# Performance work log

Measured on AMD Instinct MI355X. Metric: run time of the kernel, lower is better.

The kernel has to match this reference:

```python
import jax, jax.numpy as jnp
import numpy as np

M = 8          # ensemble size
B = 16384      # batch
HIST = 5       # history
L = 384        # latent_dim
A = 1          # action_dim
HID = 512      # hidden_dim
NHL = 2        # num_hidden_layers
DIN = L * HIST + A * HIST  # 1925
EPS = 1e-5     # BatchNorm eps


def setup_inputs() -> dict:
    key = jax.random.key(0)
    ks = jax.random.split(key, 6)
    w = lambda k, shape: (jax.random.normal(k, shape, jnp.float32) * 0.02)
    return {
        "z_hist": jax.random.normal(ks[0], (B, HIST, L), jnp.float32),
        "a_hist": jax.random.normal(ks[1], (B, HIST, A), jnp.float32),
        # per-model parameters, stacked along leading ensemble dim M
        "W1": w(ks[2], (M, DIN, HID)),
        "b1": jnp.zeros((M, HID), jnp.float32),
        "Wh": w(ks[3], (NHL, M, HID, HID)),
        "bh": jnp.zeros((NHL, M, HID), jnp.float32),
        "gamma": jnp.ones((NHL, M, HID), jnp.float32),
        "beta": jnp.zeros((NHL, M, HID), jnp.float32),
        "rmean": jnp.zeros((NHL, M, HID), jnp.float32),   # BN running mean (eval mode)
        "rvar": jnp.ones((NHL, M, HID), jnp.float32),      # BN running var (eval mode)
        "W3": w(ks[4], (M, HID, L)),
        "b3": jnp.zeros((M, L), jnp.float32),
    }


def reference(z_hist, a_hist, W1, b1, Wh, bh, gamma, beta, rmean, rvar, W3, b3):
    # EnsembleTransitionModel.forward, batched over the ensemble dim instead of
    # a Python loop over models. BatchNorm in eval mode; Dropout inactive (eval).
    bsz = z_hist.shape[0]
    x = jnp.concatenate([z_hist.reshape(bsz, -1), a_hist.reshape(bsz, -1)], axis=1)  # [B, DIN]
    # input projection + ReLU: [M, B, HID]
    h = jax.nn.relu(jnp.einsum('bi,mih->mbh', x, W1) + b1[:, None, :])
    n_layers = Wh.shape[0]
    for l in range(n_layers):  # small fixed structural loop (num_hidden_layers)
        h = jnp.einsum('mbh,mhk->mbk', h, Wh[l]) + bh[l][:, None, :]
        h = (h - rmean[l][:, None, :]) * jax.lax.rsqrt(rvar[l][:, None, :] + EPS)
        h = jax.nn.relu(h * gamma[l][:, None, :] + beta[l][:, None, :])
    delta = jnp.einsum('mbh,mhl->mbl', h, W3) + b3[:, None, :]
    # residual: pred_z = z_t + delta, broadcast over ensemble dim
    return delta + z_hist[:, -1, :][None, :, :]
```

## Files before the change

### kernel.cpp

```cpp
#include <hip/hip_runtime.h>
#include <hip/hip_bf16.h>

#define M_ENS 8
#define BATCH 16384
#define HIST 5
#define LDIM 384
#define HID 512
#define NHL 2
#define DIN 1925
#define KP 1984
#define ZLEN (HIST * LDIM)

typedef unsigned short u16;
typedef unsigned int u32;
typedef unsigned long long u64;
typedef __attribute__((ext_vector_type(8))) short bf16x8;
typedef __attribute__((ext_vector_type(4))) float f32x4;

__device__ __forceinline__ u16 f2b(float f) {
    u32 u = __builtin_bit_cast(u32, f);
    u32 r = (u + 0x7fffu + ((u >> 16) & 1u)) >> 16;
    return (u16)r;
}

#define BARRIER asm volatile("s_barrier" ::: "memory")
#define GLL(src, dst) __builtin_amdgcn_global_load_lds( \
    (const __attribute__((address_space(1))) void*)(src), \
    (__attribute__((address_space(3))) void*)(dst), 16, 0, 0)

__global__ void build_x(const float* __restrict__ z, const float* __restrict__ a,
                        u16* __restrict__ xp) {
    int idx = blockIdx.x * 256 + threadIdx.x;
    int b = idx / (KP / 4);
    int k4 = (idx % (KP / 4)) * 4;
    if (b >= BATCH) return;
    u16 r[4];
    if (k4 + 4 <= ZLEN) {
        float4 v = *(const float4*)(z + (size_t)b * ZLEN + k4);
        r[0] = f2b(v.x); r[1] = f2b(v.y); r[2] = f2b(v.z); r[3] = f2b(v.w);
    } else {
#pragma unroll
        for (int j = 0; j < 4; ++j) {
            int k = k4 + j;
            float v = 0.f;
            if (k < ZLEN)      v = z[(size_t)b * ZLEN + k];
            else if (k < DIN)  v = a[b * HIST + (k - ZLEN)];
            r[j] = f2b(v);
        }
    }
    u64 pk = (u64)r[0] | ((u64)r[1] << 16) | ((u64)r[2] << 32) | ((u64)r[3] << 48);
    *(u64*)(&xp[(size_t)b * KP + k4]) = pk;
}

__global__ void transpose_cvt(const float* __restrict__ in, u16* __restrict__ out,
                              int R, int C, int Rp) {
    __shared__ float tile[32][33];
    const float* inb = in + (size_t)blockIdx.z * R * C;
    u16* outb = out + (size_t)blockIdx.z * C * Rp;
    int r0 = blockIdx.x * 32, c0 = blockIdx.y * 32;
    int tx = threadIdx.x & 31, ty = threadIdx.x >> 5;
#pragma unroll
    for (int i = 0; i < 32; i += 8) {
        int r = r0 + ty + i;
        float v = 0.f;
        if (r < R) v = inb[(size_t)r * C + c0 + tx];
        tile[ty + i][tx] = v;
    }
    __syncthreads();
#pragma unroll
    for (int i = 0; i < 32; i += 8) {
        outb[(size_t)(c0 + ty + i) * Rp + r0 + tx] = f2b(tile[tx][ty + i]);
    }
}

__global__ void make_tables(const float* __restrict__ bh, const float* __restrict__ gamma,
                            const float* __restrict__ beta, const float* __restrict__ rmean,
                            const float* __restrict__ rvar, float* __restrict__ s,
                            float* __restrict__ t, int n) {
    int i = blockIdx.x * 256 + threadIdx.x;
    if (i >= n) return;
    float inv = rsqrtf(rvar[i] + 1e-5f);
    float sc = gamma[i] * inv;
    s[i] = sc;
    t[i] = (bh[i] - rmean[i]) * sc + beta[i];
}

__global__ __launch_bounds__(256, 4) void l1_bt(
    const u16* __restrict__ xp, const u16* __restrict__ W1t,
    const float* __restrict__ b1, u16* __restrict__ Ho) {
    __shared__ u16 As[128 * 64];
    __shared__ u16 Bs[128 * 64];

    const int tid = threadIdx.x;
    const int lane = tid & 63;
    const int wid = tid >> 6;
    const int wr = (wid >> 1) * 64;
    const int wc = (wid & 1) * 64;

    const int bid = blockIdx.x;
    const int xcd = bid & 7, i = bid >> 3;
    const int colT = xcd * 4 + (i & 3);
    const int rowT = i >> 2;
    const int rowBase = rowT * 128;
    const int colBase = colT * 128;

    const u16* Ab = xp + (size_t)rowBase * KP;
    const u16* Bb = W1t + (size_t)colBase * KP;

    f32x4 acc[4][4] = {};

    int aoff[4], boff[4];
#pragma unroll
    for (int f = 0; f < 4; ++f) {
        int ar = wr + f * 16 + (lane & 15);
        aoff[f] = (ar * 128 + ((lane >> 4) * 16)) ^ ((ar & 7) << 4);
        int br = wc + f * 16 + (lane & 15);
        boff[f] = (br * 128 + ((lane >> 4) * 16)) ^ ((br & 7) << 4);
    }

    for (int k0 = 0; k0 < KP; k0 += 64) {
#pragma unroll
        for (int s = 0; s < 4; ++s) {
            int gg = s * 256 + tid;
            int row = gg >> 3, gc = gg & 7;
            const u16* srcA = Ab + (size_t)row * KP + k0 + ((gc ^ (row & 7)) << 3);
            GLL(srcA, As + gg * 8);
            const u16* srcB = Bb + (size_t)row * KP + k0 + ((gc ^ (row & 7)) << 3);
            GLL(srcB, Bs + gg * 8);
        }
        __syncthreads();
#pragma unroll
        for (int kk = 0; kk < 2; ++kk) {
            bf16x8 af[4], bfr[4];
#pragma unroll
            for (int f = 0; f < 4; ++f) {
                af[f]  = *(const bf16x8*)((const char*)As + (aoff[f] ^ (kk << 6)));
                bfr[f] = *(const bf16x8*)((const char*)Bs + (boff[f] ^ (kk << 6)));
            }
#pragma unroll
            for (int a = 0; a < 4; ++a)
#pragma unroll
                for (int b = 0; b < 4; ++b)
                    acc[a][b] = __builtin_amdgcn_mfma_f32_16x16x32_bf16(af[a], bfr[b], acc[a][b], 0, 0, 0);
        }
        __syncthreads();
    }

#pragma unroll
    for (int a = 0; a < 4; ++a) {
        int rbase = rowBase + wr + a * 16 + ((lane >> 4) << 2);
#pragma unroll
        for (int b = 0; b < 4; ++b) {
            int c = colBase + wc + b * 16 + (lane & 15);
            float tb = b1[c];
            size_t base = (size_t)(c >> 9) * BATCH * HID + (c & 511);
#pragma unroll
            for (int q = 0; q < 4; ++q) {
                float v = acc[a][b][q] + tb;
                Ho[base + (size_t)(rbase + q) * HID] = f2b(v > 0.f ? v : 0.f);
            }
        }
    }
}

template <int MODE>
__global__ __launch_bounds__(512, 2) void gemm8p(
    const u16* __restrict__ A, const u16* __restrict__ Bw,
    const float* __restrict__ Sv, const float* __restrict__ Tv,
    u16* __restrict__ Ho, int K) {
    extern __shared__ char smem[];
    const int tid = threadIdx.x;
    const int lane = tid & 63;
    const int wid = tid >> 6;
    const int wm = wid >> 2;
    const int wn = wid & 3;

    const int nwg = gridDim.x;
    const int swz = (blockIdx.x & 7) * (nwg >> 3) + (blockIdx.x >> 3);
    const int mI = swz >> 7;
    const int rem = swz & 127;
    const int rowT = rem >> 1, colT = rem & 1;
    const u16* Ab = A + (size_t)mI * BATCH * HID;
    const u16* Bb = Bw + (size_t)mI * HID * HID + (size_t)colT * 256 * HID;
    const int lda = HID, ldb = HID;
    const int rowBase = rowT * 256;
    const int NT = K >> 6;

    auto STAGE = [&](int par, int op, int half, int tk) {
#pragma unroll
        for (int i = 0; i < 2; ++i) {
            int ii = wid * 2 + i;
            int row = ii * 8 + (lane >> 3);
            int gc = lane & 7;
            const u16* src;
            if (op == 0)
                src = Ab + (size_t)(rowBase + half * 128 + row) * lda + tk * 64 + ((gc ^ (row & 7)) << 3);
            else
                src = Bb + (size_t)(half * 128 + row) * ldb + tk * 64 + ((gc ^ (row & 7)) << 3);
            u16* dst = (u16*)(smem + par * 65536 + op * 32768 + half * 16384) + (size_t)(ii * 64 + lane) * 8;
            GLL(src, dst);
        }
    };

    const int laneRow = lane & 15;
    int xg[2];
    xg[0] = (((lane >> 4)) ^ (lane & 7)) << 4;
    xg[1] = ((4 | (lane >> 4)) ^ (lane & 7)) << 4;
#define RDF(base, r, kk) (*(const bf16x8*)((base) + (size_t)(r) * 128 + xg[kk]))

    f32x4 acc[8][4] = {};
    bf16x8 af[4][2], bfr[4][2];
    const int bcol0 = (wn & 1) * 64;

    STAGE(0, 1, 0, 0); STAGE(0, 1, 1, 0);
    STAGE(0, 0, 0, 0); STAGE(0, 0, 1, 0);
    if (NT > 1) { STAGE(1, 1, 0, 1); STAGE(1, 1, 1, 1); }
    asm volatile("s_waitcnt vmcnt(4)" ::: "memory");
    BARRIER;

    for (int T = 0; T < NT; ++T) {
        const int p = T & 1;
        const char* pA = smem + p * 65536 + wm * 16384;
        const char* pB = smem + p * 65536 + 32768 + (wn >> 1) * 16384;

#pragma unroll
        for (int mf = 0; mf < 4; ++mf) {
            af[mf][0] = RDF(pA, mf * 16 + laneRow, 0);
            af[mf][1] = RDF(pA, mf * 16 + laneRow, 1);
        }
#pragma unroll
        for (int nf = 0; nf < 2; ++nf) {
            bfr[nf][0] = RDF(pB, bcol0 + nf * 16 + laneRow, 0);
            bfr[nf][1] = RDF(pB, bcol0 + nf * 16 + laneRow, 1);
        }
        if (T + 1 < NT) STAGE((T + 1) & 1, 0, 0, T + 1);
        BARRIER;
        __builtin_amdgcn_s_setprio(1);
#pragma unroll
        for (int kk = 0; kk < 2; ++kk)
#pragma unroll
            for (int mf = 0; mf < 4; ++mf)
#pragma unroll
                for (int nf = 0; nf < 2; ++nf)
                    acc[mf][nf] = __builtin_amdgcn_mfma_f32_16x16x32_bf16(af[mf][kk], bfr[nf][kk], acc[mf][nf], 0, 0, 0);
        __builtin_amdgcn_s_setprio(0);
        BARRIER;

#pragma unroll
        for (int nf = 2; nf < 4; ++nf) {
            bfr[nf][0] = RDF(pB, bcol0 + nf * 16 + laneRow, 0);
            bfr[nf][1] = RDF(pB, bcol0 + nf * 16 + laneRow, 1);
        }
        if (T + 1 < NT) STAGE((T + 1) & 1, 0, 1, T + 1);
        BARRIER;
        __builtin_amdgcn_s_setprio(1);
#pragma unroll
        for (int kk = 0; kk < 2; ++kk)
#pragma unroll
            for (int mf = 0; mf < 4; ++mf)
#pragma unroll
                for (int nf = 2; nf < 4; ++nf)
                    acc[mf][nf] = __builtin_amdgcn_mfma_f32_16x16x32_bf16(af[mf][kk], bfr[nf][kk], acc[mf][nf], 0, 0, 0);
        __builtin_amdgcn_s_setprio(0);
        BARRIER;

#pragma unroll
        for (int mf = 0; mf < 4; ++mf) {
            af[mf][0] = RDF(pA, (4 + mf) * 16 + laneRow, 0);
            af[mf][1] = RDF(pA, (4 + mf) * 16 + laneRow, 1);
        }
        if (T + 2 < NT) STAGE(p, 1, 0, T + 2);
        BARRIER;
        __builtin_amdgcn_s_setprio(1);
#pragma unroll
        for (int kk = 0; kk < 2; ++kk)
#pragma unroll
            for (int mf = 0; mf < 4; ++mf)
#pragma unroll
                for (int nf = 2; nf < 4; ++nf)
                    acc[4 + mf][nf] = __builtin_amdgcn_mfma_f32_16x16x32_bf16(af[mf][kk], bfr[nf][kk], acc[4 + mf][nf], 0, 0, 0);
        __builtin_amdgcn_s_setprio(0);
        BARRIER;

        if (T + 2 < NT) {
            STAGE(p, 1, 1, T + 2);
            asm volatile("s_waitcnt vmcnt(4)" ::: "memory");
        } else {
            asm volatile("s_waitcnt vmcnt(0)" ::: "memory");
        }
        BARRIER;
        __builtin_amdgcn_s_setprio(1);
#pragma unroll
        for (int kk = 0; kk < 2; ++kk)
#pragma unroll
            for (int mf = 0; mf < 4; ++mf)
#pragma unroll
                for (int nf = 0; nf < 2; ++nf)
                    acc[4 + mf][nf] = __builtin_amdgcn_mfma_f32_16x16x32_bf16(af[mf][kk], bfr[nf][kk], acc[4 + mf][nf], 0, 0, 0);
        __builtin_amdgcn_s_setprio(0);
        BARRIER;
    }

#pragma unroll
    for (int mf = 0; mf < 8; ++mf) {
        int row = rowBase + wm * 128 + mf * 16 + ((lane >> 4) << 2);
#pragma unroll
        for (int nf = 0; nf < 4; ++nf) {
            int c = colT * 256 + wn * 64 + nf * 16 + (lane & 15);
            float sc = Sv[mI * HID + c], tb = Tv[mI * HID + c];
            u16* H = Ho + (size_t)mI * BATCH * HID;
#pragma unroll
            for (int q = 0; q < 4; ++q) {
                float v = acc[mf][nf][q] * sc + tb;
                H[(size_t)(row + q) * HID + c] = f2b(v > 0.f ? v : 0.f);
            }
        }
    }
}

__global__ __launch_bounds__(512, 1) void h2out(
    const u16* __restrict__ h1, const u16* __restrict__ Wh2,
    const float* __restrict__ Sv, const float* __restrict__ Tv,
    const u16* __restrict__ W3p, const float* __restrict__ b3,
    const float* __restrict__ zres, float* __restrict__ out) {
    extern __shared__ char smem[];
    const int tid = threadIdx.x;
    const int lane = tid & 63;
    const int wid = tid >> 6;
    const int wm = wid >> 2;
    const int wn = wid & 3;
    const int m = blockIdx.x & 7;
    const int rowBase = (blockIdx.x >> 3) * 128;
    const int lr15 = lane & 15;
    const int kg = lane >> 4;

    const u16* Ab = h1 + ((size_t)m * BATCH + rowBase) * HID;
    const u16* Bb = Wh2 + (size_t)m * HID * HID;
    const u16* W3b = W3p + (size_t)m * LDIM * HID;
    const float* b3b = b3 + m * LDIM;

    int xg[2];
    xg[0] = (((lane >> 4)) ^ (lane & 7)) << 4;
    xg[1] = ((4 | (lane >> 4)) ^ (lane & 7)) << 4;

    auto stA = [&](int par, int tk) {
#pragma unroll
        for (int i = 0; i < 2; ++i) {
            int ii = wid * 2 + i;
            int row = ii * 8 + (lane >> 3);
            int gc = lane & 7;
            const u16* src = Ab + (size_t)row * HID + tk * 64 + ((gc ^ (row & 7)) << 3);
            u16* dst = (u16*)(smem + par * 16384) + (size_t)(ii * 64 + lane) * 8;
            GLL(src, dst);
        }
    };
    auto stB = [&](int par, int q, int tk) {
#pragma unroll
        for (int i = 0; i < 2; ++i) {
            int ii = wid * 2 + i;
            int row = ii * 8 + (lane >> 3);
            int gc = lane & 7;
            const u16* src = Bb + (size_t)(q * 128 + row) * HID + tk * 64 + ((gc ^ (row & 7)) << 3);
            u16* dst = (u16*)(smem + 32768 + par * 65536 + q * 16384) + (size_t)(ii * 64 + lane) * 8;
            GLL(src, dst);
        }
    };

    f32x4 acc[4][8] = {};
    bf16x8 afr[4][2];
    const int NT = HID / 64;

    stA(0, 0); stB(0, 0, 0); stB(0, 1, 0); stB(0, 2, 0); stB(0, 3, 0);
    asm volatile("s_waitcnt vmcnt(0)" ::: "memory");
    BARRIER;

    for (int T = 0; T < NT; ++T) {
        const int p = T & 1;
        const char* pA = smem + p * 16384;
        const char* qb = smem + 32768 + p * 65536 + wn * 16384;

#pragma unroll
        for (int mf = 0; mf < 4; ++mf) {
            int lr = wm * 64 + mf * 16 + lr15;
            afr[mf][0] = RDF(pA, lr, 0);
            afr[mf][1] = RDF(pA, lr, 1);
        }
        bf16x8 b01[2][2];
#pragma unroll
        for (int nf = 0; nf < 2; ++nf) {
            b01[nf][0] = RDF(qb, nf * 16 + lr15, 0);
            b01[nf][1] = RDF(qb, nf * 16 + lr15, 1);
        }
        if (T + 1 < NT) stA(p ^ 1, T + 1);
        BARRIER;
        __builtin_amdgcn_s_setprio(1);
#pragma unroll
        for (int kk = 0; kk < 2; ++kk)
#pragma unroll
            for (int mf = 0; mf < 4; ++mf)
#pragma unroll
                for (int nf = 0; nf < 2; ++nf)
                    acc[mf][nf] = __builtin_amdgcn_mfma_f32_16x16x32_bf16(afr[mf][kk], b01[nf][kk], acc[mf][nf], 0, 0, 0);
        __builtin_amdgcn_s_setprio(0);
        BARRIER;

#pragma unroll
        for (int nf = 0; nf < 2; ++nf) {
            b01[nf][0] = RDF(qb, (2 + nf) * 16 + lr15, 0);
            b01[nf][1] = RDF(qb, (2 + nf) * 16 + lr15, 1);
        }
        if (T + 1 < NT) { stB(p ^ 1, 0, T + 1); stB(p ^ 1, 1, T + 1); }
        BARRIER;
        __builtin_amdgcn_s_setprio(1);
#pragma unroll
        for (int kk = 0; kk < 2; ++kk)
#pragma unroll
            for (int mf = 0; mf < 4; ++mf)
#pragma unroll
                for (int nf = 0; nf < 2; ++nf)
                    acc[mf][2 + nf] = __builtin_amdgcn_mfma_f32_16x16x32_bf16(afr[mf][kk], b01[nf][kk], acc[mf][2 + nf], 0, 0, 0);
        __builtin_amdgcn_s_setprio(0);
        BARRIER;

#pragma unroll
        for (int nf = 0; nf < 2; ++nf) {
            b01[nf][0] = RDF(qb, (4 + nf) * 16 + lr15, 0);
            b01[nf][1] = RDF(qb, (4 + nf) * 16 + lr15, 1);
        }
        if (T + 1 < NT) { stB(p ^ 1, 2, T + 1); stB(p ^ 1, 3, T + 1); }
        BARRIER;
        __builtin_amdgcn_s_setprio(1);
#pragma unroll
        for (int kk = 0; kk < 2; ++kk)
#pragma unroll
            for (int mf = 0; mf < 4; ++mf)
#pragma unroll
                for (int nf = 0; nf < 2; ++nf)
                    acc[mf][4 + nf] = __builtin_amdgcn_mfma_f32_16x16x32_bf16(afr[mf][kk], b01[nf][kk], acc[mf][4 + nf], 0, 0, 0);
        __builtin_amdgcn_s_setprio(0);
        BARRIER;

#pragma unroll
        for (int nf = 0; nf < 2; ++nf) {
            b01[nf][0] = RDF(qb, (6 + nf) * 16 + lr15, 0);
            b01[nf][1] = RDF(qb, (6 + nf) * 16 + lr15, 1);
        }
        if (T + 2 < NT) {
            stA(p, T + 2);
            asm volatile("s_waitcnt vmcnt(2)" ::: "memory");
        } else {
            asm volatile("s_waitcnt vmcnt(0)" ::: "memory");
        }
        BARRIER;
        __builtin_amdgcn_s_setprio(1);
#pragma unroll
        for (int kk = 0; kk < 2; ++kk)
#pragma unroll
            for (int mf = 0; mf < 4; ++mf)
#pragma unroll
                for (int nf = 0; nf < 2; ++nf)
                    acc[mf][6 + nf] = __builtin_amdgcn_mfma_f32_16x16x32_bf16(afr[mf][kk], b01[nf][kk], acc[mf][6 + nf], 0, 0, 0);
        __builtin_amdgcn_s_setprio(0);
        BARRIER;
    }

#pragma unroll
    for (int mf = 0; mf < 4; ++mf) {
#pragma unroll
        for (int nf = 0; nf < 8; ++nf) {
            int col = wn * 128 + nf * 16 + lr15;
            float sc = Sv[m * HID + col], tt = Tv[m * HID + col];
#pragma unroll
            for (int q = 0; q < 4; ++q) {
                int row = wm * 64 + mf * 16 + ((lane >> 4) << 2) + q;
                float v = acc[mf][nf][q] * sc + tt;
                v = v > 0.f ? v : 0.f;
                *(u16*)(smem + 32768 + row * 1024 + (((col >> 3) ^ (row & 7)) << 4) + ((col & 7) << 1)) = f2b(v);
            }
        }
    }
    asm volatile("s_waitcnt lgkmcnt(0)" ::: "memory");
    BARRIER;

    f32x4 acc2[4][6] = {};
    for (int t = 0; t < 16; ++t) {
        bf16x8 a1[4], b1r[6];
#pragma unroll
        for (int nf = 0; nf < 6; ++nf) {
            int r3 = wn * 96 + nf * 16 + lr15;
            b1r[nf] = *(const bf16x8*)(W3b + (size_t)r3 * HID + t * 32 + kg * 8);
        }
#pragma unroll
        for (int mf = 0; mf < 4; ++mf) {
            int r = wm * 64 + mf * 16 + lr15;
            a1[mf] = *(const bf16x8*)(smem + 32768 + r * 1024 + (((4 * t + kg) ^ (r & 7)) << 4));
        }
#pragma unroll
        for (int mf = 0; mf < 4; ++mf)
#pragma unroll
            for (int nf = 0; nf < 6; ++nf)
                acc2[mf][nf] = __builtin_amdgcn_mfma_f32_16x16x32_bf16(a1[mf], b1r[nf], acc2[mf][nf], 0, 0, 0);
    }

#pragma unroll
    for (int mf = 0; mf < 4; ++mf) {
#pragma unroll
        for (int nf = 0; nf < 6; ++nf) {
            int c = wn * 96 + nf * 16 + lr15;
            float bv = b3b[c];
#pragma unroll
            for (int q = 0; q < 4; ++q) {
                int grow = rowBase + wm * 64 + mf * 16 + ((lane >> 4) << 2) + q;
                out[((size_t)m * BATCH + grow) * LDIM + c] =
                    acc2[mf][nf][q] + bv + zres[(size_t)grow * (HIST * LDIM) + (HIST - 1) * LDIM + c];
            }
        }
    }
}

template <int MODE>
__global__ __launch_bounds__(256, 2) void gemm_bt(
    const u16* __restrict__ A, size_t aStride, int lda,
    const u16* __restrict__ Bt, size_t bStride,
    const float* __restrict__ Sv, const float* __restrict__ Tv, int ptStride,
    u16* __restrict__ Ho, size_t hStride,
    float* __restrict__ Fo, size_t fStride,
    const float* __restrict__ Zres,
    int K, int m0) {
    __shared__ u16 As[128 * 64];
    __shared__ u16 Bs[128 * 64];

    const int tid = threadIdx.x;
    const int lane = tid & 63;
    const int wid = tid >> 6;
    const int wr = (wid >> 1) * 64;
    const int wc = (wid & 1) * 64;
    const int z = blockIdx.z;
    const int rowBase = blockIdx.x * 128;
    const int colBase = blockIdx.y * 128;

    const u16* Ab = A + (size_t)z * aStride;
    const u16* Bb = Bt + (size_t)z * bStride;

    f32x4 acc[4][4] = {};

    int aoff[4], boff[4];
#pragma unroll
    for (int f = 0; f < 4; ++f) {
        int ar = wr + f * 16 + (lane & 15);
        aoff[f] = (ar * 128 + ((lane >> 4) * 16)) ^ ((ar & 7) << 4);
        int br = wc + f * 16 + (lane & 15);
        boff[f] = (br * 128 + ((lane >> 4) * 16)) ^ ((br & 7) << 4);
    }

    for (int k0 = 0; k0 < K; k0 += 64) {
#pragma unroll
        for (int i = 0; i < 4; ++i) {
            int gg = i * 256 + tid;
            int row = gg >> 3, gc = gg & 7;
            const u16* srcA = Ab + (size_t)(rowBase + row) * lda + k0 + ((gc ^ (row & 7)) << 3);
            GLL(srcA, As + gg * 8);
            const u16* srcB = Bb + (size_t)(colBase + row) * K + k0 + ((gc ^ (row & 7)) << 3);
            GLL(srcB, Bs + gg * 8);
        }
        __syncthreads();
#pragma unroll
        for (int kk = 0; kk < 2; ++kk) {
            bf16x8 af[4], bfr[4];
#pragma unroll
            for (int f = 0; f < 4; ++f) {
                af[f]  = *(const bf16x8*)((const char*)As + (aoff[f] ^ (kk << 6)));
                bfr[f] = *(const bf16x8*)((const char*)Bs + (boff[f] ^ (kk << 6)));
            }
#pragma unroll
            for (int i = 0; i < 4; ++i)
#pragma unroll
                for (int j = 0; j < 4; ++j)
                    acc[i][j] = __builtin_amdgcn_mfma_f32_16x16x32_bf16(af[i], bfr[j], acc[i][j], 0, 0, 0);
        }
        __syncthreads();
    }

    const int mg = m0 + z;
#pragma unroll
    for (int i = 0; i < 4; ++i) {
        int rbase = rowBase + wr + i * 16 + ((lane >> 4) << 2);
#pragma unroll
        for (int j = 0; j < 4; ++j) {
            int n = colBase + wc + j * 16 + (lane & 15);
            if (MODE == 0) {
                float bias = Tv[(size_t)mg * ptStride + n];
                u16* H = Ho + (size_t)z * hStride;
#pragma unroll
                for (int q = 0; q < 4; ++q) {
                    float v = acc[i][j][q] + bias;
                    v = v > 0.f ? v : 0.f;
                    H[(size_t)(rbase + q) * HID + n] = f2b(v);
                }
            } else if (MODE == 1) {
                float sc = Sv[(size_t)mg * ptStride + n];
                float tt = Tv[(size_t)mg * ptStride + n];
                u16* H = Ho + (size_t)z * hStride;
#pragma unroll
                for (int q = 0; q < 4; ++q) {
                    float v = acc[i][j][q] * sc + tt;
                    v = v > 0.f ? v : 0.f;
                    H[(size_t)(rbase + q) * HID + n] = f2b(v);
                }
            } else {
                float bias = Tv[(size_t)mg * ptStride + n];
                float* F = Fo + (size_t)z * fStride;
#pragma unroll
                for (int q = 0; q < 4; ++q) {
                    int b = rbase + q;
                    float v = acc[i][j][q] + bias + Zres[(size_t)b * (HIST * LDIM) + (HIST - 1) * LDIM + n];
                    F[(size_t)b * LDIM + n] = v;
                }
            }
        }
    }
}

extern "C" void kernel_launch(void* const* d_in, const int* in_sizes, int n_in,
                              void* d_out, int out_size, void* d_ws, size_t ws_size,
                              hipStream_t stream) {
    const float* z_hist = (const float*)d_in[0];
    const float* a_hist = (const float*)d_in[1];
    const float* W1    = (const float*)d_in[2];
    const float* b1    = (const float*)d_in[3];
    const float* Wh    = (const float*)d_in[4];
    const float* bh    = (const float*)d_in[5];
    const float* gamma = (const float*)d_in[6];
    const float* beta  = (const float*)d_in[7];
    const float* rmean = (const float*)d_in[8];
    const float* rvar  = (const float*)d_in[9];
    const float* W3    = (const float*)d_in[10];
    const float* b3    = (const float*)d_in[11];
    float* out = (float*)d_out;

    char* ws = (char*)d_ws;
    size_t off = 0;
    auto alloc = [&](size_t bytes) {
        void* p = ws + off;
        off = (off + bytes + 255) & ~(size_t)255;
        return p;
    };
    u16* xp  = (u16*)alloc((size_t)BATCH * KP * 2);
    u16* W1t = (u16*)alloc((size_t)M_ENS * HID * KP * 2);
    u16* Wht = (u16*)alloc((size_t)NHL * M_ENS * HID * HID * 2);
    u16* W3t = (u16*)alloc((size_t)M_ENS * LDIM * HID * 2);
    float* stab = (float*)alloc((size_t)NHL * M_ENS * HID * 4);
    float* ttab = (float*)alloc((size_t)NHL * M_ENS * HID * 4);
    size_t fixed = off;
    size_t hFull = (size_t)M_ENS * BATCH * HID * 2;
    bool full = (fixed + 2 * hFull <= ws_size);
    int MC = full ? M_ENS : 1;
    u16* h0 = (u16*)alloc((size_t)MC * BATCH * HID * 2);
    u16* h1 = (u16*)alloc((size_t)MC * BATCH * HID * 2);

    {
        int total = BATCH * KP / 4;
        build_x<<<(total + 255) / 256, 256, 0, stream>>>(z_hist, a_hist, xp);
        dim3 g1(KP / 32, HID / 32, M_ENS);
        transpose_cvt<<<g1, 256, 0, stream>>>(W1, W1t, DIN, HID, KP);
        dim3 g2(HID / 32, HID / 32, NHL * M_ENS);
        transpose_cvt<<<g2, 256, 0, stream>>>(Wh, Wht, HID, HID, HID);
        dim3 g3(HID / 32, LDIM / 32, M_ENS);
        transpose_cvt<<<g3, 256, 0, stream>>>(W3, W3t, HID, LDIM, HID);
        int n = NHL * M_ENS * HID;
        make_tables<<<(n + 255) / 256, 256, 0, stream>>>(bh, gamma, beta, rmean, rvar, stab, ttab, n);
    }

    if (full) {
        (void)hipFuncSetAttribute(reinterpret_cast<const void*>(&gemm8p<1>),
                                  hipFuncAttributeMaxDynamicSharedMemorySize, 131072);
        (void)hipFuncSetAttribute(reinterpret_cast<const void*>(&h2out),
                                  hipFuncAttributeMaxDynamicSharedMemorySize, 163840);
        l1_bt<<<4096, 256, 0, stream>>>(xp, W1t, b1, h0);
        gemm8p<1><<<1024, 512, 131072, stream>>>(h0, Wht, stab, ttab, h1, HID);
        h2out<<<1024, 512, 163840, stream>>>(
            h1, Wht + (size_t)M_ENS * HID * HID,
            stab + M_ENS * HID, ttab + M_ENS * HID,
            W3t, b3, z_hist, out);
    } else {
        for (int m0 = 0; m0 < M_ENS; m0 += MC) {
            dim3 grid(BATCH / 128, HID / 128, MC);
            gemm_bt<0><<<grid, 256, 0, stream>>>(
                xp, 0, KP,
                W1t + (size_t)m0 * HID * KP, (size_t)HID * KP,
                nullptr, b1, HID,
                h0, (size_t)BATCH * HID, nullptr, 0, nullptr,
                KP, m0);
            for (int l = 0; l < NHL; ++l) {
                u16* hin = l ? h1 : h0;
                u16* hout = l ? h0 : h1;
                gemm_bt<1><<<grid, 256, 0, stream>>>(
                    hin, (size_t)BATCH * HID, HID,
                    Wht + ((size_t)l * M_ENS + m0) * HID * HID, (size_t)HID * HID,
                    stab + (size_t)l * M_ENS * HID, ttab + (size_t)l * M_ENS * HID, HID,
                    hout, (size_t)BATCH * HID, nullptr, 0, nullptr,
                    HID, m0);
            }
            dim3 gridO(BATCH / 128, LDIM / 128, MC);
            gemm_bt<2><<<gridO, 256, 0, stream>>>(
                h0, (size_t)BATCH * HID, HID,
                W3t + (size_t)m0 * LDIM * HID, (size_t)LDIM * HID,
                nullptr, b3, LDIM,
                nullptr, 0,
                out + (size_t)m0 * BATCH * LDIM, (size_t)BATCH * LDIM,
                z_hist,
                HID, 0);
        }
    }
}
```

Measured before the change: 636.8 us.

## Halve h2out row tile, stream Wh2 from global, raise occupancy

The fused layer-2 plus output kernel now processes 64 rows per block instead of 128, launching twice as many blocks. It drops LDS staging of the Wh2 weight tiles and reads B fragments straight from global/L2, so shared memory shrinks to 80KB and launch bounds allow up to 4 blocks per SM. The goal is higher occupancy and less barrier-heavy pipelining, at the cost of more global weight traffic per block and unhidden load latency on the B reads.

```diff
diff --git a/kernel.cpp b/kernel.cpp
--- a/kernel.cpp
+++ b/kernel.cpp
@@ -318,7 +318,7 @@
     }
 }
 
-__global__ __launch_bounds__(512, 1) void h2out(
+__global__ __launch_bounds__(512, 4) void h2out(
     const u16* __restrict__ h1, const u16* __restrict__ Wh2,
     const float* __restrict__ Sv, const float* __restrict__ Tv,
     const u16* __restrict__ W3p, const float* __restrict__ b3,
@@ -330,7 +330,7 @@
     const int wm = wid >> 2;
     const int wn = wid & 3;
     const int m = blockIdx.x & 7;
-    const int rowBase = (blockIdx.x >> 3) * 128;
+    const int rowBase = (blockIdx.x >> 3) * 64;
     const int lr15 = lane & 15;
     const int kg = lane >> 4;
 
@@ -344,173 +344,93 @@
     xg[1] = ((4 | (lane >> 4)) ^ (lane & 7)) << 4;
 
     auto stA = [&](int par, int tk) {
-#pragma unroll
-        for (int i = 0; i < 2; ++i) {
-            int ii = wid * 2 + i;
-            int row = ii * 8 + (lane >> 3);
-            int gc = lane & 7;
-            const u16* src = Ab + (size_t)row * HID + tk * 64 + ((gc ^ (row & 7)) << 3);
-            u16* dst = (u16*)(smem + par * 16384) + (size_t)(ii * 64 + lane) * 8;
-            GLL(src, dst);
-        }
+        int row = tid >> 3, gc = tid & 7;
+        const u16* src = Ab + (size_t)row * HID + tk * 64 + ((gc ^ (row & 7)) << 3);
+        GLL(src, (u16*)(smem + par * 8192) + tid * 8);
     };
-    auto stB = [&](int par, int q, int tk) {
-#pragma unroll
-        for (int i = 0; i < 2; ++i) {
-            int ii = wid * 2 + i;
-            int row = ii * 8 + (lane >> 3);
-            int gc = lane & 7;
-            const u16* src = Bb + (size_t)(q * 128 + row) * HID + tk * 64 + ((gc ^ (row & 7)) << 3);
-            u16* dst = (u16*)(smem + 32768 + par * 65536 + q * 16384) + (size_t)(ii * 64 + lane) * 8;
-            GLL(src, dst);
-        }
-    };
-
-    f32x4 acc[4][8] = {};
-    bf16x8 afr[4][2];
+
+    f32x4 acc[2][8] = {};
     const int NT = HID / 64;
 
-    stA(0, 0); stB(0, 0, 0); stB(0, 1, 0); stB(0, 2, 0); stB(0, 3, 0);
+    stA(0, 0);
     asm volatile("s_waitcnt vmcnt(0)" ::: "memory");
     BARRIER;
 
     for (int T = 0; T < NT; ++T) {
         const int p = T & 1;
-        const char* pA = smem + p * 16384;
-        const char* qb = smem + 32768 + p * 65536 + wn * 16384;
-
-#pragma unroll
-        for (int mf = 0; mf < 4; ++mf) {
-            int lr = wm * 64 + mf * 16 + lr15;
-            afr[mf][0] = RDF(pA, lr, 0);
-            afr[mf][1] = RDF(pA, lr, 1);
-        }
-        bf16x8 b01[2][2];
-#pragma unroll
-        for (int nf = 0; nf < 2; ++nf) {
-            b01[nf][0] = RDF(qb, nf * 16 + lr15, 0);
-            b01[nf][1] = RDF(qb, nf * 16 + lr15, 1);
+        const char* pA = smem + p * 8192;
+
+        bf16x8 afr[2][2];
+#pragma unroll
+        for (int mf = 0; mf < 2; ++mf) {
+            int r = wm * 32 + mf * 16 + lr15;
+            afr[mf][0] = RDF(pA, r, 0);
+            afr[mf][1] = RDF(pA, r, 1);
         }
         if (T + 1 < NT) stA(p ^ 1, T + 1);
-        BARRIER;
-        __builtin_amdgcn_s_setprio(1);
-#pragma unroll
-        for (int kk = 0; kk < 2; ++kk)
-#pragma unroll
-            for (int mf = 0; mf < 4; ++mf)
-#pragma unroll
-                for (int nf = 0; nf < 2; ++nf)
-                    acc[mf][nf] = __builtin_amdgcn_mfma_f32_16x16x32_bf16(afr[mf][kk], b01[nf][kk], acc[mf][nf], 0, 0, 0);
-        __builtin_amdgcn_s_setprio(0);
-        BARRIER;
-
-#pragma unroll
-        for (int nf = 0; nf < 2; ++nf) {
-            b01[nf][0] = RDF(qb, (2 + nf) * 16 + lr15, 0);
-            b01[nf][1] = RDF(qb, (2 + nf) * 16 + lr15, 1);
-        }
-        if (T + 1 < NT) { stB(p ^ 1, 0, T + 1); stB(p ^ 1, 1, T + 1); }
-        BARRIER;
-        __builtin_amdgcn_s_setprio(1);
-#pragma unroll
-        for (int kk = 0; kk < 2; ++kk)
-#pragma unroll
-            for (int mf = 0; mf < 4; ++mf)
-#pragma unroll
-                for (int nf = 0; nf < 2; ++nf)
-                    acc[mf][2 + nf] = __builtin_amdgcn_mfma_f32_16x16x32_bf16(afr[mf][kk], b01[nf][kk], acc[mf][2 + nf], 0, 0, 0);
-        __builtin_amdgcn_s_setprio(0);
-        BARRIER;
-
-#pragma unroll
-        for (int nf = 0; nf < 2; ++nf) {
-            b01[nf][0] = RDF(qb, (4 + nf) * 16 + lr15, 0);
-            b01[nf][1] = RDF(qb, (4 + nf) * 16 + lr15, 1);
-        }
-        if (T + 1 < NT) { stB(p ^ 1, 2, T + 1); stB(p ^ 1, 3, T + 1); }
-        BARRIER;
-        __builtin_amdgcn_s_setprio(1);
-#pragma unroll
-        for (int kk = 0; kk < 2; ++kk)
-#pragma unroll
-            for (int mf = 0; mf < 4; ++mf)
-#pragma unroll
-                for (int nf = 0; nf < 2; ++nf)
-                    acc[mf][4 + nf] = __builtin_amdgcn_mfma_f32_16x16x32_bf16(afr[mf][kk], b01[nf][kk], acc[mf][4 + nf], 0, 0, 0);
-        __builtin_amdgcn_s_setprio(0);
-        BARRIER;
-
-#pragma unroll
-        for (int nf = 0; nf < 2; ++nf) {
-            b01[nf][0] = RDF(qb, (6 + nf) * 16 + lr15, 0);
-            b01[nf][1] = RDF(qb, (6 + nf) * 16 + lr15, 1);
-        }
-        if (T + 2 < NT) {
-            stA(p, T + 2);
-            asm volatile("s_waitcnt vmcnt(2)" ::: "memory");
-        } else {
-            asm volatile("s_waitcnt vmcnt(0)" ::: "memory");
-        }
-        BARRIER;
-        __builtin_amdgcn_s_setprio(1);
-#pragma unroll
-        for (int kk = 0; kk < 2; ++kk)
-#pragma unroll
-            for (int mf = 0; mf < 4; ++mf)
-#pragma unroll
-                for (int nf = 0; nf < 2; ++nf)
-                    acc[mf][6 + nf] = __builtin_amdgcn_mfma_f32_16x16x32_bf16(afr[mf][kk], b01[nf][kk], acc[mf][6 + nf], 0, 0, 0);
-        __builtin_amdgcn_s_setprio(0);
-        BARRIER;
-    }
-
-#pragma unroll
-    for (int mf = 0; mf < 4; ++mf) {
+
+        const u16* bbase = Bb + (size_t)(wn * 128 + lr15) * HID + T * 64 + kg * 8;
+#pragma unroll
+        for (int nf = 0; nf < 8; ++nf) {
+            bf16x8 b0 = *(const bf16x8*)(bbase + (size_t)nf * 16 * HID);
+            bf16x8 b1v = *(const bf16x8*)(bbase + (size_t)nf * 16 * HID + 32);
+#pragma unroll
+            for (int mf = 0; mf < 2; ++mf) {
+                acc[mf][nf] = __builtin_amdgcn_mfma_f32_16x16x32_bf16(afr[mf][0], b0, acc[mf][nf], 0, 0, 0);
+                acc[mf][nf] = __builtin_amdgcn_mfma_f32_16x16x32_bf16(afr[mf][1], b1v, acc[mf][nf], 0, 0, 0);
+            }
+        }
+        asm volatile("s_waitcnt vmcnt(0)" ::: "memory");
+        BARRIER;
+    }
+
+#pragma unroll
+    for (int mf = 0; mf < 2; ++mf) {
 #pragma unroll
         for (int nf = 0; nf < 8; ++nf) {
             int col = wn * 128 + nf * 16 + lr15;
             float sc = Sv[m * HID + col], tt = Tv[m * HID + col];
 #pragma unroll
             for (int q = 0; q < 4; ++q) {
-                int row = wm * 64 + mf * 16 + ((lane >> 4) << 2) + q;
+                int row = wm * 32 + mf * 16 + (kg << 2) + q;
                 float v = acc[mf][nf][q] * sc + tt;
                 v = v > 0.f ? v : 0.f;
-                *(u16*)(smem + 32768 + row * 1024 + (((col >> 3) ^ (row & 7)) << 4) + ((col & 7) << 1)) = f2b(v);
+                *(u16*)(smem + 16384 + row * 1024 + (((col >> 3) ^ (row & 7)) << 4) + ((col & 7) << 1)) = f2b(v);
             }
         }
     }
     asm volatile("s_waitcnt lgkmcnt(0)" ::: "memory");
     BARRIER;
 
-    f32x4 acc2[4][6] = {};
+    f32x4 acc2[2][6] = {};
     for (int t = 0; t < 16; ++t) {
-        bf16x8 a1[4], b1r[6];
+        bf16x8 a1[2], b1r[6];
 #pragma unroll
         for (int nf = 0; nf < 6; ++nf) {
             int r3 = wn * 96 + nf * 16 + lr15;
             b1r[nf] = *(const bf16x8*)(W3b + (size_t)r3 * HID + t * 32 + kg * 8);
         }
 #pragma unroll
-        for (int mf = 0; mf < 4; ++mf) {
-            int r = wm * 64 + mf * 16 + lr15;
-            a1[mf] = *(const bf16x8*)(smem + 32768 + r * 1024 + (((4 * t + kg) ^ (r & 7)) << 4));
-        }
-#pragma unroll
-        for (int mf = 0; mf < 4; ++mf)
+        for (int mf = 0; mf < 2; ++mf) {
+            int r = wm * 32 + mf * 16 + lr15;
+            a1[mf] = *(const bf16x8*)(smem + 16384 + r * 1024 + (((4 * t + kg) ^ (r & 7)) << 4));
+        }
+#pragma unroll
+        for (int mf = 0; mf < 2; ++mf)
 #pragma unroll
             for (int nf = 0; nf < 6; ++nf)
                 acc2[mf][nf] = __builtin_amdgcn_mfma_f32_16x16x32_bf16(a1[mf], b1r[nf], acc2[mf][nf], 0, 0, 0);
     }
 
 #pragma unroll
-    for (int mf = 0; mf < 4; ++mf) {
+    for (int mf = 0; mf < 2; ++mf) {
 #pragma unroll
         for (int nf = 0; nf < 6; ++nf) {
             int c = wn * 96 + nf * 16 + lr15;
             float bv = b3b[c];
 #pragma unroll
             for (int q = 0; q < 4; ++q) {
-                int grow = rowBase + wm * 64 + mf * 16 + ((lane >> 4) << 2) + q;
+                int grow = rowBase + wm * 32 + mf * 16 + (kg << 2) + q;
                 out[((size_t)m * BATCH + grow) * LDIM + c] =
                     acc2[mf][nf][q] + bv + zres[(size_t)grow * (HIST * LDIM) + (HIST - 1) * LDIM + c];
             }
@@ -675,10 +595,10 @@
         (void)hipFuncSetAttribute(reinterpret_cast<const void*>(&gemm8p<1>),
                                   hipFuncAttributeMaxDynamicSharedMemorySize, 131072);
         (void)hipFuncSetAttribute(reinterpret_cast<const void*>(&h2out),
-                                  hipFuncAttributeMaxDynamicSharedMemorySize, 163840);
+                                  hipFuncAttributeMaxDynamicSharedMemorySize, 81920);
         l1_bt<<<4096, 256, 0, stream>>>(xp, W1t, b1, h0);
         gemm8p<1><<<1024, 512, 131072, stream>>>(h0, Wht, stab, ttab, h1, HID);
-        h2out<<<1024, 512, 163840, stream>>>(
+        h2out<<<2048, 512, 81920, stream>>>(
             h1, Wht + (size_t)M_ENS * HID * HID,
             stab + M_ENS * HID, ttab + M_ENS * HID,
             W3t, b3, z_hist, out);
```

Result: slower. 871.8 us (+36.9%).
